# Kernel tuning notes

Hardware: AMD Instinct MI355X
Metric: run time of the kernel (lower is better)

## Reference

```python
import jax, jax.numpy as jnp
import numpy as np

D, E, K, H = 512, 8, 2, 128   # input_dim, num_experts, top-k, expert hidden (Expert default)
CAPF = 1.25                    # capacity_factor
N = 32768                      # tokens


def setup_inputs() -> dict:
    key = jax.random.key(0)
    ks = jax.random.split(key, 6)
    s = 0.02
    return {
        "x":  jax.random.normal(ks[0], (N, D), jnp.float32),
        "Wr": jax.random.normal(ks[1], (D, E), jnp.float32) * s,   # router linear weight
        "br": jnp.zeros((E,), jnp.float32),
        "W1": jax.random.normal(ks[2], (E, D, H), jnp.float32) * s,  # expert first linear (stacked)
        "b1": jnp.zeros((E, H), jnp.float32),
        "W2": jax.random.normal(ks[3], (E, H, D), jnp.float32) * s,  # expert second linear (stacked)
        "b2": jnp.zeros((E, D), jnp.float32),
    }


def reference(x, Wr, br, W1, b1, W2, b2):
    n = x.shape[0]
    # ---- router (eval mode: no noise, temperature=1) ----
    logits = x @ Wr + br                                   # [N, E]
    topk_vals, topk_idx = jax.lax.top_k(logits, K)         # [N, K]
    gates_k = jax.nn.softmax(topk_vals, axis=-1)
    rows = jnp.arange(n)[:, None]
    sparse_gates = jnp.zeros_like(logits).at[rows, topk_idx].set(gates_k)  # [N, E]
    confidence = topk_vals.max(axis=-1).mean()
    # ---- capacity-limited dispatch (keep first `cap` routed tokens per expert) ----
    cap = int(CAPF * (n / E))
    mask = sparse_gates > 0                                # [N, E] routed mask
    pos = jnp.cumsum(mask, axis=0) - 1                     # rank of token within expert queue
    keep = mask & (pos < cap)                              # [N, E]
    load = keep.sum(axis=0).astype(x.dtype)                # [E]
    # ---- per-expert 2-layer FFN over all tokens, combined with keep mask ----
    # (original adds expert output un-weighted by gates to kept token positions)
    h = jax.nn.relu(jnp.einsum('nd,edh->enh', x, W1) + b1[:, None, :])   # [E, N, H]
    y = jnp.einsum('enh,ehd->end', h, W2) + b2[:, None, :]               # [E, N, D]
    out = jnp.einsum('ne,end->nd', keep.astype(x.dtype), y)             # [N, D]
    # ---- load-balance stats ----
    load_dist = load / (load.sum() + 1e-8)
    load_loss = (load_dist * jnp.log(load_dist + 1e-8)).sum()
    return out, load_loss, load_dist, confidence
```

## Files before the change

kernel.cpp:

```cpp
#include <hip/hip_runtime.h>

#define D 512
#define E 8
#define H 128
#define BM 64
#define HP 136
#define RT 16

typedef __attribute__((ext_vector_type(8))) short short8v;
typedef __attribute__((ext_vector_type(4))) short short4v;
typedef __attribute__((ext_vector_type(4))) float float4v;

__device__ inline short f2bf(float f) {
  union { float f; unsigned u; } v; v.f = f;
  unsigned r = v.u + 0x7fffu + ((v.u >> 16) & 1u);
  return (short)(r >> 16);
}
__device__ inline float bf2f(short s) {
  union { unsigned u; float f; } v;
  v.u = ((unsigned)(unsigned short)s) << 16;
  return v.f;
}

__global__ void k_swizzle(const float* __restrict__ W1, const float* __restrict__ W2,
                          short* __restrict__ W1f, short* __restrict__ W2f) {
  const int e = blockIdx.y;
  const int lane = threadIdx.x & 63;
  const int wv = threadIdx.x >> 6;
  const int r = lane & 15, g = lane >> 4;
  const int which = blockIdx.x >> 4;
  const int fbase = ((blockIdx.x & 15) * 4 + wv) * 2;
  if (which == 0) {
#pragma unroll
    for (int f = fbase; f < fbase + 2; ++f) {
      int ks = f >> 3, t = f & 7;
      const float* src = W1 + ((size_t)e * D + ks * 32 + g * 8) * H + t * 16 + r;
      short8v o;
#pragma unroll
      for (int j = 0; j < 8; ++j) o[j] = f2bf(src[(size_t)j * H]);
      *(short8v*)(W1f + (((size_t)e * 128 + f) * 64 + lane) * 8) = o;
    }
  } else {
#pragma unroll
    for (int f = fbase; f < fbase + 2; ++f) {
      int ks = f >> 5, t = f & 31;
      const float* src = W2 + ((size_t)e * H + ks * 32 + g * 8) * D + t * 16 + r;
      short8v o;
#pragma unroll
      for (int j = 0; j < 8; ++j) o[j] = f2bf(src[(size_t)j * D]);
      *(short8v*)(W2f + (((size_t)e * 128 + f) * 64 + lane) * 8) = o;
    }
  }
}

__global__ void k_router(const float* __restrict__ x, const float* __restrict__ Wr,
                         const float* __restrict__ br, int* __restrict__ tokE,
                         float* __restrict__ confPart, short* __restrict__ xb) {
  const int lane = threadIdx.x & 63;
  const int wave = threadIdx.x >> 6;
  const int tbase = (blockIdx.x * 4 + wave) * RT;

  float wr[8][8];
  const float4* wrp = reinterpret_cast<const float4*>(Wr) + lane * 16;
#pragma unroll
  for (int j = 0; j < 8; ++j) {
    float4 a = wrp[j * 2 + 0];
    float4 b = wrp[j * 2 + 1];
    wr[j][0] = a.x; wr[j][1] = a.y; wr[j][2] = a.z; wr[j][3] = a.w;
    wr[j][4] = b.x; wr[j][5] = b.y; wr[j][6] = b.z; wr[j][7] = b.w;
  }

  const int myE = ((lane & 1) << 2) | (lane & 2) | ((lane >> 2) & 1);
  const float brv = br[myE];

  float conf = 0.f;

#pragma unroll 2
  for (int tt = 0; tt < RT; ++tt) {
    const int token = tbase + tt;
    const float4* xp = reinterpret_cast<const float4*>(x + (size_t)token * D + lane * 8);
    float4 x0 = xp[0], x1 = xp[1];
    float xv[8] = {x0.x, x0.y, x0.z, x0.w, x1.x, x1.y, x1.z, x1.w};

    if (xb) {
      short8v p;
#pragma unroll
      for (int j = 0; j < 8; ++j) p[j] = f2bf(xv[j]);
      *(short8v*)(xb + (size_t)token * D + lane * 8) = p;
    }

    float v[8] = {0, 0, 0, 0, 0, 0, 0, 0};
#pragma unroll
    for (int j = 0; j < 8; ++j)
#pragma unroll
      for (int e = 0; e < E; ++e)
        v[e] += xv[j] * wr[j][e];

#pragma unroll
    for (int i = 0; i < 4; ++i) {
      float a = v[i] + __shfl_xor(v[i], 1, 64);
      float b = v[i + 4] + __shfl_xor(v[i + 4], 1, 64);
      v[i] = (lane & 1) ? b : a;
    }
#pragma unroll
    for (int i = 0; i < 2; ++i) {
      float a = v[i] + __shfl_xor(v[i], 2, 64);
      float b = v[i + 2] + __shfl_xor(v[i + 2], 2, 64);
      v[i] = (lane & 2) ? b : a;
    }
    {
      float a = v[0] + __shfl_xor(v[0], 4, 64);
      float b = v[1] + __shfl_xor(v[1], 4, 64);
      v[0] = (lane & 4) ? b : a;
    }
    v[0] += __shfl_xor(v[0], 8, 64);
    v[0] += __shfl_xor(v[0], 16, 64);
    v[0] += __shfl_xor(v[0], 32, 64);

    const float logit = v[0] + brv;

    float m1 = logit; int i1 = myE;
#pragma unroll
    for (int m = 1; m <= 4; m <<= 1) {
      float om = __shfl_xor(m1, m, 64);
      int oi = __shfl_xor(i1, m, 64);
      bool take = (om > m1) || (om == m1 && oi < i1);
      m1 = take ? om : m1;
      i1 = take ? oi : i1;
    }
    float s1 = (myE == i1) ? -1e30f : logit; int j1 = myE;
#pragma unroll
    for (int m = 1; m <= 4; m <<= 1) {
      float om = __shfl_xor(s1, m, 64);
      int oi = __shfl_xor(j1, m, 64);
      bool take = (om > s1) || (om == s1 && oi < j1);
      s1 = take ? om : s1;
      j1 = take ? oi : j1;
    }

    if (lane == 0) {
      tokE[token * 2 + 0] = i1;
      tokE[token * 2 + 1] = j1;
    }
    conf += m1;
  }

  __shared__ float cf[4];
  if (lane == 0) cf[wave] = conf;
  __syncthreads();
  if (threadIdx.x == 0) confPart[blockIdx.x] = cf[0] + cf[1] + cf[2] + cf[3];
}

__global__ void k_count(const int* __restrict__ tokE, int* __restrict__ chunkCnt) {
  __shared__ int c[E];
  if (threadIdx.x < E) c[threadIdx.x] = 0;
  __syncthreads();
  int token = blockIdx.x * 256 + threadIdx.x;
  atomicAdd(&c[tokE[token * 2 + 0]], 1);
  atomicAdd(&c[tokE[token * 2 + 1]], 1);
  __syncthreads();
  if (threadIdx.x < E) chunkCnt[blockIdx.x * E + threadIdx.x] = c[threadIdx.x];
}

__global__ void k_scan(const int* __restrict__ chunkCnt, const float* __restrict__ confPart,
                       int* __restrict__ chunkOff, int* __restrict__ kept,
                       float* __restrict__ outTail, int nConf, int cap, int nTok) {
  const int lane = threadIdx.x & 63;
  const int e = threadIdx.x >> 6;
  __shared__ int keptS[E];

  int v0 = chunkCnt[lane * E + e];
  int v1 = chunkCnt[(64 + lane) * E + e];
  int s0 = v0, s1 = v1;
#pragma unroll
  for (int off = 1; off < 64; off <<= 1) {
    int t0 = __shfl_up(s0, off, 64);
    int t1 = __shfl_up(s1, off, 64);
    if (lane >= off) { s0 += t0; s1 += t1; }
  }
  int tot0 = __shfl(s0, 63, 64);
  int total = tot0 + __shfl(s1, 63, 64);
  chunkOff[lane * E + e] = s0 - v0;
  chunkOff[(64 + lane) * E + e] = tot0 + s1 - v1;
  if (lane == 0) {
    int k = min(total, cap);
    kept[e] = k;
    keptS[e] = k;
  }

  __shared__ float s[512];
  float a = 0.f;
  for (int i = threadIdx.x; i < nConf; i += 512) a += confPart[i];
  s[threadIdx.x] = a;
  __syncthreads();
  for (int st = 256; st > 0; st >>= 1) {
    if (threadIdx.x < st) s[threadIdx.x] += s[threadIdx.x + st];
    __syncthreads();
  }
  if (threadIdx.x == 0) {
    float tot = 0.f, ld[E];
    for (int i = 0; i < E; ++i) { ld[i] = (float)keptS[i]; tot += ld[i]; }
    float denom = tot + 1e-8f;
    float loss = 0.f;
    for (int i = 0; i < E; ++i) {
      float dist = ld[i] / denom;
      loss += dist * logf(dist + 1e-8f);
      outTail[1 + i] = dist;
    }
    outTail[0] = loss;
    outTail[1 + E] = s[0] / (float)nTok;
  }
}

__global__ void k_dispatch(const int* __restrict__ tokE, const int* __restrict__ chunkOff,
                           int* __restrict__ expList, int2* __restrict__ tokSlot, int cap) {
  const int lane = threadIdx.x & 63;
  const int wave = threadIdx.x >> 6;
  const int token = blockIdx.x * 256 + threadIdx.x;
  const int e0 = tokE[token * 2 + 0];
  const int e1 = tokE[token * 2 + 1];
  __shared__ int wcnt[4][E];
  unsigned long long lt = (lane == 63) ? 0x7fffffffffffffffull : ((1ull << lane) - 1ull);
  int r0 = 0, r1 = 0;
#pragma unroll
  for (int e = 0; e < E; ++e) {
    unsigned long long b0 = __ballot(e0 == e);
    unsigned long long b1 = __ballot(e1 == e);
    unsigned long long m = b0 | b1;
    if (e0 == e) r0 = __popcll(m & lt);
    if (e1 == e) r1 = __popcll(m & lt);
    if (lane == 0) wcnt[wave][e] = __popcll(m);
  }
  __syncthreads();
  int base0 = chunkOff[blockIdx.x * E + e0];
  int base1 = chunkOff[blockIdx.x * E + e1];
  for (int w = 0; w < wave; ++w) {
    base0 += wcnt[w][e0];
    base1 += wcnt[w][e1];
  }
  int g0 = base0 + r0;
  int g1 = base1 + r1;
  if (g0 < cap) expList[e0 * cap + g0] = token;
  if (g1 < cap) expList[e1 * cap + g1] = token;
  tokSlot[token] = make_int2(g0 < cap ? e0 * cap + g0 : -1,
                             g1 < cap ? e1 * cap + g1 : -1);
}

template <bool USE_XB>
__global__ __launch_bounds__(256, 1) void k_expert_mfma(
    const short* __restrict__ xb, const float* __restrict__ x,
    const short* __restrict__ W1f, const float* __restrict__ b1,
    const short* __restrict__ W2f, const float* __restrict__ b2,
    const int* __restrict__ expList, const int* __restrict__ kept,
    short* __restrict__ yscr, int cap) {
  const int e = blockIdx.y;
  const int cnt = kept[e];
  const int t0 = blockIdx.x * BM;
  if (t0 >= cnt) return;
  const int lane = threadIdx.x & 63;
  const int wave = threadIdx.x >> 6;
  const int rb = wave * 16;
  const int n15 = lane & 15;
  const int grp = lane >> 4;
  const int kg = grp * 8;

  __shared__ int toks[BM];
  __shared__ short hs[BM][HP];

  if (threadIdx.x < BM) {
    int idx = min(t0 + (int)threadIdx.x, cnt - 1);
    toks[threadIdx.x] = expList[e * cap + idx];
  }
  __syncthreads();

  short8v xf[16];
  if (USE_XB) {
    const short* xrow = xb + (size_t)toks[rb + n15] * D + kg;
#pragma unroll
    for (int ks = 0; ks < 16; ++ks)
      xf[ks] = *(const short8v*)(xrow + ks * 32);
  } else {
    const float* xrow = x + (size_t)toks[rb + n15] * D + kg;
#pragma unroll
    for (int ks = 0; ks < 16; ++ks) {
      float4 a = *(const float4*)(xrow + ks * 32);
      float4 b = *(const float4*)(xrow + ks * 32 + 4);
      short8v f;
      f[0] = f2bf(a.x); f[1] = f2bf(a.y); f[2] = f2bf(a.z); f[3] = f2bf(a.w);
      f[4] = f2bf(b.x); f[5] = f2bf(b.y); f[6] = f2bf(b.z); f[7] = f2bf(b.w);
      xf[ks] = f;
    }
  }

  const short* w1 = W1f + ((size_t)e * 128 * 64 + lane) * 8;
  float4v acc[8];
#pragma unroll
  for (int t = 0; t < 8; ++t) acc[t] = (float4v){0.f, 0.f, 0.f, 0.f};
#pragma unroll
  for (int ks = 0; ks < 16; ++ks) {
    short8v wf[8];
#pragma unroll
    for (int t = 0; t < 8; ++t)
      wf[t] = *(const short8v*)(w1 + (size_t)(ks * 8 + t) * 64 * 8);
#pragma unroll
    for (int t = 0; t < 8; ++t)
      acc[t] = __builtin_amdgcn_mfma_f32_16x16x32_bf16(wf[t], xf[ks], acc[t], 0, 0, 0);
  }
#pragma unroll
  for (int t = 0; t < 8; ++t) {
    float4 bb = *(const float4*)(b1 + e * H + t * 16 + grp * 4);
    short4v p;
    p[0] = f2bf(fmaxf(acc[t][0] + bb.x, 0.f));
    p[1] = f2bf(fmaxf(acc[t][1] + bb.y, 0.f));
    p[2] = f2bf(fmaxf(acc[t][2] + bb.z, 0.f));
    p[3] = f2bf(fmaxf(acc[t][3] + bb.w, 0.f));
    *(short4v*)(&hs[rb + n15][t * 16 + grp * 4]) = p;
  }
  __syncthreads();

  short8v a4[4];
#pragma unroll
  for (int ks = 0; ks < 4; ++ks)
    a4[ks] = *(const short8v*)(&hs[rb + n15][ks * 32 + kg]);

  const short* w2 = W2f + ((size_t)e * 128 * 64 + lane) * 8;
  short* yrow = yscr + ((size_t)(e * cap + t0 + rb + n15)) * D;
#pragma unroll 4
  for (int t = 0; t < 32; ++t) {
    short8v wf[4];
#pragma unroll
    for (int ks = 0; ks < 4; ++ks)
      wf[ks] = *(const short8v*)(w2 + (size_t)(ks * 32 + t) * 64 * 8);
    float4v y = (float4v){0.f, 0.f, 0.f, 0.f};
#pragma unroll
    for (int ks = 0; ks < 4; ++ks)
      y = __builtin_amdgcn_mfma_f32_16x16x32_bf16(wf[ks], a4[ks], y, 0, 0, 0);
    float4 bb = *(const float4*)(b2 + e * D + t * 16 + grp * 4);
    short4v p;
    p[0] = f2bf(y[0] + bb.x);
    p[1] = f2bf(y[1] + bb.y);
    p[2] = f2bf(y[2] + bb.z);
    p[3] = f2bf(y[3] + bb.w);
    *(short4v*)(yrow + t * 16 + grp * 4) = p;
  }
}

__global__ void k_combine(const short* __restrict__ yscr, const int2* __restrict__ tokSlot,
                          float* __restrict__ out) {
  const int idx = blockIdx.x * 256 + threadIdx.x;
  const int token = idx >> 7;
  const int c4 = idx & 127;
  int2 sl = tokSlot[token];
  float4 r = make_float4(0.f, 0.f, 0.f, 0.f);
  if (sl.x >= 0) {
    short4v y = *(const short4v*)(yscr + (size_t)sl.x * D + c4 * 4);
    r.x += bf2f(y[0]); r.y += bf2f(y[1]); r.z += bf2f(y[2]); r.w += bf2f(y[3]);
  }
  if (sl.y >= 0) {
    short4v y = *(const short4v*)(yscr + (size_t)sl.y * D + c4 * 4);
    r.x += bf2f(y[0]); r.y += bf2f(y[1]); r.z += bf2f(y[2]); r.w += bf2f(y[3]);
  }
  reinterpret_cast<float4*>(out)[idx] = r;
}

extern "C" void kernel_launch(void* const* d_in, const int* in_sizes, int n_in,
                              void* d_out, int out_size, void* d_ws, size_t ws_size,
                              hipStream_t stream) {
  const float* x  = (const float*)d_in[0];
  const float* Wr = (const float*)d_in[1];
  const float* br = (const float*)d_in[2];
  const float* W1 = (const float*)d_in[3];
  const float* b1 = (const float*)d_in[4];
  const float* W2 = (const float*)d_in[5];
  const float* b2 = (const float*)d_in[6];
  float* out = (float*)d_out;

  const int N = in_sizes[0] / D;
  const int cap = (int)(1.25f * (float)(N / E));
  const int chunks = N / 256;
  const int rblocks = N / (4 * RT);

  int* tokE = (int*)d_ws;
  float* confPart = (float*)(tokE + (size_t)N * 2);
  int* chunkCnt = (int*)(confPart + rblocks);
  int* chunkOff = chunkCnt + chunks * E;
  int* kept = chunkOff + chunks * E;
  int2* tokSlot = (int2*)(kept + E);
  int* expList = (int*)(tokSlot + N);
  short* W1f = (short*)(expList + (size_t)E * cap);
  short* W2f = W1f + (size_t)E * H * D;
  short* yscr = W2f + (size_t)E * H * D;
  short* xb = yscr + (size_t)E * cap * D;

  const size_t needed = (size_t)((char*)(xb + (size_t)N * D) - (char*)d_ws);
  const bool useXB = ws_size >= needed;

  k_swizzle<<<dim3(32, E), 256, 0, stream>>>(W1, W2, W1f, W2f);

  k_router<<<rblocks, 256, 0, stream>>>(x, Wr, br, tokE, confPart,
                                        useXB ? xb : nullptr);
  k_count<<<chunks, 256, 0, stream>>>(tokE, chunkCnt);
  k_scan<<<1, 512, 0, stream>>>(chunkCnt, confPart, chunkOff, kept,
                                out + (size_t)N * D, rblocks, cap, N);
  k_dispatch<<<chunks, 256, 0, stream>>>(tokE, chunkOff, expList, tokSlot, cap);

  const int tiles = (cap + BM - 1) / BM;
  dim3 g5(tiles, E);
  if (useXB)
    k_expert_mfma<true><<<g5, 256, 0, stream>>>(xb, x, W1f, b1, W2f, b2,
                                                expList, kept, yscr, cap);
  else
    k_expert_mfma<false><<<g5, 256, 0, stream>>>(nullptr, x, W1f, b1, W2f, b2,
                                                 expList, kept, yscr, cap);

  k_combine<<<(N * D / 4) / 256, 256, 0, stream>>>(yscr, tokSlot, out);
}
```

Measured before the change: 113.8 us.

## Stage expert weights through double-buffered LDS via async global_load_lds

Expert FFN weight fragments are now loaded cooperatively into a double-buffered shared-memory tile with global_load_lds, prefetching the next chunk while MFMAs consume the current one. Before, each wave read every weight fragment directly from global memory. W2 is reswizzled so each chunk is contiguous in t-major order. This cuts redundant per-wave global weight traffic across the four waves, at the cost of 32KB more LDS per block, which may lower occupancy, plus a barrier per chunk.

```diff
diff --git a/kernel.cpp b/kernel.cpp
--- a/kernel.cpp
+++ b/kernel.cpp
@@ -20,6 +20,11 @@
   union { unsigned u; float f; } v;
   v.u = ((unsigned)(unsigned short)s) << 16;
   return v.f;
+}
+__device__ inline void gload_lds16(const void* g, void* l) {
+  __builtin_amdgcn_global_load_lds(
+      (const __attribute__((address_space(1))) unsigned int*)g,
+      (__attribute__((address_space(3))) unsigned int*)l, 16, 0, 0);
 }
 
 __global__ void k_swizzle(const float* __restrict__ W1, const float* __restrict__ W2,
@@ -43,7 +48,7 @@
   } else {
 #pragma unroll
     for (int f = fbase; f < fbase + 2; ++f) {
-      int ks = f >> 5, t = f & 31;
+      int t = f >> 2, ks = f & 3;
       const float* src = W2 + ((size_t)e * H + ks * 32 + g * 8) * D + t * 16 + r;
       short8v o;
 #pragma unroll
@@ -266,11 +271,23 @@
 
   __shared__ int toks[BM];
   __shared__ short hs[BM][HP];
+  __shared__ short wbuf[2][8192];
+
+  auto stage = [&](const short* wset, int b, int buf) {
+    const short* src = wset + ((size_t)(b * 16 + wave * 4) * 64 + lane) * 8;
+    short* dst = &wbuf[buf][(wave * 4) * 512];
+#pragma unroll
+    for (int j = 0; j < 4; ++j)
+      gload_lds16(src + (size_t)j * 512, dst + j * 512);
+  };
 
   if (threadIdx.x < BM) {
     int idx = min(t0 + (int)threadIdx.x, cnt - 1);
     toks[threadIdx.x] = expList[e * cap + idx];
   }
+  const short* w1 = W1f + (size_t)e * 128 * 512;
+  const short* w2 = W2f + (size_t)e * 128 * 512;
+  stage(w1, 0, 0);
   __syncthreads();
 
   short8v xf[16];
@@ -292,19 +309,21 @@
     }
   }
 
-  const short* w1 = W1f + ((size_t)e * 128 * 64 + lane) * 8;
   float4v acc[8];
 #pragma unroll
   for (int t = 0; t < 8; ++t) acc[t] = (float4v){0.f, 0.f, 0.f, 0.f};
-#pragma unroll
-  for (int ks = 0; ks < 16; ++ks) {
-    short8v wf[8];
-#pragma unroll
-    for (int t = 0; t < 8; ++t)
-      wf[t] = *(const short8v*)(w1 + (size_t)(ks * 8 + t) * 64 * 8);
-#pragma unroll
-    for (int t = 0; t < 8; ++t)
-      acc[t] = __builtin_amdgcn_mfma_f32_16x16x32_bf16(wf[t], xf[ks], acc[t], 0, 0, 0);
+  int cur = 0;
+#pragma unroll 1
+  for (int b = 0; b < 8; ++b) {
+    if (b < 7) stage(w1, b + 1, cur ^ 1);
+#pragma unroll
+    for (int l = 0; l < 16; ++l) {
+      short8v wf = *(const short8v*)(&wbuf[cur][l * 512 + lane * 8]);
+      int ks = 2 * b + (l >> 3), t = l & 7;
+      acc[t] = __builtin_amdgcn_mfma_f32_16x16x32_bf16(wf, xf[ks], acc[t], 0, 0, 0);
+    }
+    __syncthreads();
+    cur ^= 1;
   }
 #pragma unroll
   for (int t = 0; t < 8; ++t) {
@@ -316,6 +335,8 @@
     p[3] = f2bf(fmaxf(acc[t][3] + bb.w, 0.f));
     *(short4v*)(&hs[rb + n15][t * 16 + grp * 4]) = p;
   }
+
+  stage(w2, 0, 0);
   __syncthreads();
 
   short8v a4[4];
@@ -323,25 +344,30 @@
   for (int ks = 0; ks < 4; ++ks)
     a4[ks] = *(const short8v*)(&hs[rb + n15][ks * 32 + kg]);
 
-  const short* w2 = W2f + ((size_t)e * 128 * 64 + lane) * 8;
   short* yrow = yscr + ((size_t)(e * cap + t0 + rb + n15)) * D;
-#pragma unroll 4
-  for (int t = 0; t < 32; ++t) {
-    short8v wf[4];
-#pragma unroll
-    for (int ks = 0; ks < 4; ++ks)
-      wf[ks] = *(const short8v*)(w2 + (size_t)(ks * 32 + t) * 64 * 8);
-    float4v y = (float4v){0.f, 0.f, 0.f, 0.f};
-#pragma unroll
-    for (int ks = 0; ks < 4; ++ks)
-      y = __builtin_amdgcn_mfma_f32_16x16x32_bf16(wf[ks], a4[ks], y, 0, 0, 0);
-    float4 bb = *(const float4*)(b2 + e * D + t * 16 + grp * 4);
-    short4v p;
-    p[0] = f2bf(y[0] + bb.x);
-    p[1] = f2bf(y[1] + bb.y);
-    p[2] = f2bf(y[2] + bb.z);
-    p[3] = f2bf(y[3] + bb.w);
-    *(short4v*)(yrow + t * 16 + grp * 4) = p;
+  cur = 0;
+#pragma unroll 1
+  for (int b = 0; b < 8; ++b) {
+    if (b < 7) stage(w2, b + 1, cur ^ 1);
+#pragma unroll
+    for (int tt = 0; tt < 4; ++tt) {
+      float4v y = (float4v){0.f, 0.f, 0.f, 0.f};
+#pragma unroll
+      for (int ks = 0; ks < 4; ++ks) {
+        short8v wf = *(const short8v*)(&wbuf[cur][(tt * 4 + ks) * 512 + lane * 8]);
+        y = __builtin_amdgcn_mfma_f32_16x16x32_bf16(wf, a4[ks], y, 0, 0, 0);
+      }
+      int t = b * 4 + tt;
+      float4 bb = *(const float4*)(b2 + e * D + t * 16 + grp * 4);
+      short4v p;
+      p[0] = f2bf(y[0] + bb.x);
+      p[1] = f2bf(y[1] + bb.y);
+      p[2] = f2bf(y[2] + bb.z);
+      p[3] = f2bf(y[3] + bb.w);
+      *(short4v*)(yrow + t * 16 + grp * 4) = p;
+    }
+    __syncthreads();
+    cur ^= 1;
   }
 }
 
```

Measured after the change: 120.4 us. 5.7% more time.

## Stage gathered x rows through LDS with double-buffered async loads

Applied to the files above, without the earlier changes.

The bf16 x path of the expert kernel no longer loads all 16 k-slices of each gathered token row into registers up front. It streams 128-column chunks into a double-buffered LDS region with global_load_lds and overlaps the next chunk's load with the current chunk's MFMAs. The W2 fragment layout is reordered so the four k-slices for one output tile sit contiguously. Dropping the occupancy hint of 1 in launch_bounds lets more blocks run per CU, at the cost of extra LDS use and barriers per chunk.

```diff
diff --git a/kernel.cpp b/kernel.cpp
--- a/kernel.cpp
+++ b/kernel.cpp
@@ -20,6 +20,11 @@
   union { unsigned u; float f; } v;
   v.u = ((unsigned)(unsigned short)s) << 16;
   return v.f;
+}
+__device__ inline void gload_lds4(const void* g, void* l) {
+  __builtin_amdgcn_global_load_lds(
+      (const __attribute__((address_space(1))) unsigned int*)g,
+      (__attribute__((address_space(3))) unsigned int*)l, 4, 0, 0);
 }
 
 __global__ void k_swizzle(const float* __restrict__ W1, const float* __restrict__ W2,
@@ -43,7 +48,7 @@
   } else {
 #pragma unroll
     for (int f = fbase; f < fbase + 2; ++f) {
-      int ks = f >> 5, t = f & 31;
+      int t = f >> 2, ks = f & 3;
       const float* src = W2 + ((size_t)e * H + ks * 32 + g * 8) * D + t * 16 + r;
       short8v o;
 #pragma unroll
@@ -247,7 +252,7 @@
 }
 
 template <bool USE_XB>
-__global__ __launch_bounds__(256, 1) void k_expert_mfma(
+__global__ __launch_bounds__(256) void k_expert_mfma(
     const short* __restrict__ xb, const float* __restrict__ x,
     const short* __restrict__ W1f, const float* __restrict__ b1,
     const short* __restrict__ W2f, const float* __restrict__ b2,
@@ -265,7 +270,7 @@
   const int kg = grp * 8;
 
   __shared__ int toks[BM];
-  __shared__ short hs[BM][HP];
+  __shared__ short sbuf[2 * BM * HP];
 
   if (threadIdx.x < BM) {
     int idx = min(t0 + (int)threadIdx.x, cnt - 1);
@@ -273,39 +278,69 @@
   }
   __syncthreads();
 
-  short8v xf[16];
+  const short* w1 = W1f + (size_t)e * (128 * 512);
+  const short* w2 = W2f + (size_t)e * (128 * 512);
+
+  float4v acc[8];
+#pragma unroll
+  for (int t = 0; t < 8; ++t) acc[t] = (float4v){0.f, 0.f, 0.f, 0.f};
+
   if (USE_XB) {
-    const short* xrow = xb + (size_t)toks[rb + n15] * D + kg;
-#pragma unroll
-    for (int ks = 0; ks < 16; ++ks)
-      xf[ks] = *(const short8v*)(xrow + ks * 32);
+    auto stageX = [&](int p) {
+#pragma unroll
+      for (int j = 0; j < 16; ++j) {
+        int ti = wave * 16 + j;
+        const short* src = xb + (size_t)toks[ti] * D + p * 128 + lane * 2;
+        short* dst = &sbuf[(p & 1) * (BM * HP) + ti * HP];
+        gload_lds4(src, dst);
+      }
+    };
+    stageX(0);
+    __syncthreads();
+#pragma unroll
+    for (int p = 0; p < 4; ++p) {
+      if (p < 3) stageX(p + 1);
+#pragma unroll
+      for (int ksl = 0; ksl < 4; ++ksl) {
+        const int ks = p * 4 + ksl;
+        short8v xf = *(const short8v*)&sbuf[(p & 1) * (BM * HP) +
+                                            (rb + n15) * HP + ksl * 32 + kg];
+        short8v wf[8];
+#pragma unroll
+        for (int t = 0; t < 8; ++t)
+          wf[t] = *(const short8v*)(w1 + (size_t)(ks * 8 + t) * 512 + lane * 8);
+#pragma unroll
+        for (int t = 0; t < 8; ++t)
+          acc[t] = __builtin_amdgcn_mfma_f32_16x16x32_bf16(wf[t], xf, acc[t], 0, 0, 0);
+      }
+      __syncthreads();
+    }
   } else {
-    const float* xrow = x + (size_t)toks[rb + n15] * D + kg;
+    const float* xrowF = x + (size_t)toks[rb + n15] * D + kg;
+    short8v xf[16];
 #pragma unroll
     for (int ks = 0; ks < 16; ++ks) {
-      float4 a = *(const float4*)(xrow + ks * 32);
-      float4 b = *(const float4*)(xrow + ks * 32 + 4);
+      float4 a = *(const float4*)(xrowF + ks * 32);
+      float4 b = *(const float4*)(xrowF + ks * 32 + 4);
       short8v f;
       f[0] = f2bf(a.x); f[1] = f2bf(a.y); f[2] = f2bf(a.z); f[3] = f2bf(a.w);
       f[4] = f2bf(b.x); f[5] = f2bf(b.y); f[6] = f2bf(b.z); f[7] = f2bf(b.w);
       xf[ks] = f;
     }
-  }
-
-  const short* w1 = W1f + ((size_t)e * 128 * 64 + lane) * 8;
-  float4v acc[8];
-#pragma unroll
-  for (int t = 0; t < 8; ++t) acc[t] = (float4v){0.f, 0.f, 0.f, 0.f};
-#pragma unroll
-  for (int ks = 0; ks < 16; ++ks) {
-    short8v wf[8];
-#pragma unroll
-    for (int t = 0; t < 8; ++t)
-      wf[t] = *(const short8v*)(w1 + (size_t)(ks * 8 + t) * 64 * 8);
-#pragma unroll
-    for (int t = 0; t < 8; ++t)
-      acc[t] = __builtin_amdgcn_mfma_f32_16x16x32_bf16(wf[t], xf[ks], acc[t], 0, 0, 0);
-  }
+#pragma unroll
+    for (int ks = 0; ks < 16; ++ks) {
+      short8v wf[8];
+#pragma unroll
+      for (int t = 0; t < 8; ++t)
+        wf[t] = *(const short8v*)(w1 + (size_t)(ks * 8 + t) * 512 + lane * 8);
+#pragma unroll
+      for (int t = 0; t < 8; ++t)
+        acc[t] = __builtin_amdgcn_mfma_f32_16x16x32_bf16(wf[t], xf[ks], acc[t], 0, 0, 0);
+    }
+    __syncthreads();
+  }
+
+  short* hrow = &sbuf[(rb + n15) * HP];
 #pragma unroll
   for (int t = 0; t < 8; ++t) {
     float4 bb = *(const float4*)(b1 + e * H + t * 16 + grp * 4);
@@ -314,23 +349,22 @@
     p[1] = f2bf(fmaxf(acc[t][1] + bb.y, 0.f));
     p[2] = f2bf(fmaxf(acc[t][2] + bb.z, 0.f));
     p[3] = f2bf(fmaxf(acc[t][3] + bb.w, 0.f));
-    *(short4v*)(&hs[rb + n15][t * 16 + grp * 4]) = p;
+    *(short4v*)(hrow + t * 16 + grp * 4) = p;
   }
   __syncthreads();
 
   short8v a4[4];
 #pragma unroll
   for (int ks = 0; ks < 4; ++ks)
-    a4[ks] = *(const short8v*)(&hs[rb + n15][ks * 32 + kg]);
-
-  const short* w2 = W2f + ((size_t)e * 128 * 64 + lane) * 8;
+    a4[ks] = *(const short8v*)(&sbuf[(rb + n15) * HP + ks * 32 + kg]);
+
   short* yrow = yscr + ((size_t)(e * cap + t0 + rb + n15)) * D;
 #pragma unroll 4
   for (int t = 0; t < 32; ++t) {
     short8v wf[4];
 #pragma unroll
     for (int ks = 0; ks < 4; ++ks)
-      wf[ks] = *(const short8v*)(w2 + (size_t)(ks * 32 + t) * 64 * 8);
+      wf[ks] = *(const short8v*)(w2 + (size_t)(t * 4 + ks) * 512 + lane * 8);
     float4v y = (float4v){0.f, 0.f, 0.f, 0.f};
 #pragma unroll
     for (int ks = 0; ks < 4; ++ks)
```

Measured after the change: 113.3 us. Within noise of the previous version (-0.5%).
